# Kernel optimization log

Measured on AMD Instinct MI355X. Metric: run time of the kernel, lower is better.

## Reference

```python
import jax, jax.numpy as jnp
import numpy as np

N, K, D = 32768, 8192, 512
COMMITMENT_COST = 0.25

def setup_inputs() -> dict:
    key = jax.random.key(0)
    k1, k2 = jax.random.split(key)
    z = jax.random.normal(k1, (N, D), dtype=jnp.float32)
    # original inits uniform(-1/K, 1/K); scaled uniform keeps same distribution
    emb_weight = jax.random.uniform(k2, (K, D), dtype=jnp.float32, minval=-1.0 / K, maxval=1.0 / K)
    return {"z": z, "emb_weight": emb_weight}

def reference(z, emb_weight):
    z_flat = z.reshape(-1, emb_weight.shape[1])  # [N, D]
    # squared L2 distances: ||z||^2 + ||e||^2 - 2 z e^T  -> [N, K]
    distances = (
        jnp.sum(z_flat ** 2, axis=1, keepdims=True)
        + jnp.sum(emb_weight ** 2, axis=1)
        - 2.0 * jnp.matmul(z_flat, emb_weight.T)
    )
    code_indices = jnp.argmin(distances, axis=1)  # [N]
    quantized = emb_weight[code_indices]          # [N, D] gather
    e_latent_loss = jnp.mean((jax.lax.stop_gradient(quantized) - z_flat) ** 2)
    q_latent_loss = jnp.mean((quantized - jax.lax.stop_gradient(z_flat)) ** 2)
    loss = q_latent_loss + COMMITMENT_COST * e_latent_loss
    # straight-through estimator
    quantized_st = z_flat + jax.lax.stop_gradient(quantized - z_flat)
    return quantized_st, loss, code_indices
```

## Files before the change

kernel.cpp:

```cpp
#include <hip/hip_runtime.h>


#define N_ROWS 32768
#define K_CODES 8192
#define DIM 512

typedef __attribute__((ext_vector_type(8))) short short8;
typedef __attribute__((ext_vector_type(4))) float f32x4;

#define MARGIN 5e-4f

__device__ __forceinline__ unsigned short f2bf(float f) {
  unsigned int u = __float_as_uint(f);
  u = u + 0x7fffu + ((u >> 16) & 1u);
  return (unsigned short)(u >> 16);
}

__device__ __forceinline__ double shfl_xor_dbl(double v, int m) {
  union { double d; int i[2]; } u;
  u.d = v;
  u.i[0] = __shfl_xor(u.i[0], m, 64);
  u.i[1] = __shfl_xor(u.i[1], m, 64);
  return u.d;
}

__device__ __forceinline__ float opaque_f(float x) {
  asm volatile("" : "+v"(x));
  return x;
}

__global__ __launch_bounds__(256) void cvtnorm_k(
    const float* __restrict__ z, const float* __restrict__ e,
    unsigned short* __restrict__ zb, unsigned short* __restrict__ eb,
    float* __restrict__ a32, float* __restrict__ b32) {
  const int r = blockIdx.x * 4 + (threadIdx.x >> 6);
  const int lane = threadIdx.x & 63;
  const float* in; unsigned short* outb; float* outn; int rr;
  if (r < N_ROWS) { in = z; outb = zb; outn = a32; rr = r; }
  else            { in = e; outb = eb; outn = b32; rr = r - N_ROWS; }
  const float* xr = in + (size_t)rr * DIM + lane * 8;
  const float4 a = *(const float4*)xr;
  const float4 b = *(const float4*)(xr + 4);
  uint4 o;
  o.x = (unsigned)f2bf(a.x) | ((unsigned)f2bf(a.y) << 16);
  o.y = (unsigned)f2bf(a.z) | ((unsigned)f2bf(a.w) << 16);
  o.z = (unsigned)f2bf(b.x) | ((unsigned)f2bf(b.y) << 16);
  o.w = (unsigned)f2bf(b.z) | ((unsigned)f2bf(b.w) << 16);
  *(uint4*)(outb + (size_t)rr * DIM + lane * 8) = o;
  double s = (double)a.x * a.x + (double)a.y * a.y + (double)a.z * a.z + (double)a.w * a.w
           + (double)b.x * b.x + (double)b.y * b.y + (double)b.z * b.z + (double)b.w * b.w;
#pragma unroll
  for (int m = 1; m < 64; m <<= 1) s += shfl_xor_dbl(s, m);
  if (lane == 0) outn[rr] = (float)s;
}

__global__ __launch_bounds__(512, 4) void gemm_topk(
    const unsigned short* __restrict__ A,
    const unsigned short* __restrict__ B,
    const float* __restrict__ en2,
    float* __restrict__ candk,
    int* __restrict__ candi)
{
  __shared__ char lds[77824];
  float* scorebuf = (float*)lds;
  float* e2sAll = (float*)(lds + 73728);

  const int tid = threadIdx.x;
  const int lane = tid & 63, wave = tid >> 6;
  const int wm = wave >> 1, wn = wave & 1;
  const int quad = lane >> 4, lcol = lane & 15;
  const int bx = blockIdx.x >> 3, by = blockIdx.x & 7;
  const int row0 = bx * 256;
  const int cstart = by * 1024;
  const int hf = tid & 1, srow = tid >> 1;

  e2sAll[tid] = en2[cstart + tid];
  e2sAll[tid + 512] = en2[cstart + 512 + tid];

  float tk0 = 3.4e38f, tk1 = 3.4e38f, tk2 = 3.4e38f, tk3 = 3.4e38f;
  int ti0 = 0, ti1 = 0, ti2 = 0, ti3 = 0;

  const int schm = (lane & 3) ^ ((lane >> 3) & 3);
  const unsigned short* Ag =
      A + ((size_t)(row0 + wave * 32 + (lane >> 2))) * DIM + schm * 8;
  const int dstA = wave * 2048;
  const int dstB = 16384 + wave * 1024;

  const int swz = (quad ^ ((lcol >> 1) & 3)) * 16;
  int aoff[4], boff[4];
#pragma unroll
  for (int i = 0; i < 4; ++i) aoff[i] = (wm * 64 + i * 16 + lcol) * 64 + swz;
#pragma unroll
  for (int j = 0; j < 4; ++j) boff[j] = 16384 + (wn * 64 + j * 16 + lcol) * 64 + swz;

#define ASGP const __attribute__((address_space(1))) void*
#define LDSP __attribute__((address_space(3))) void*
#define STAGE(ktv, bb) do {                                                        \
    const unsigned short* As_ = Ag + (ktv) * 32;                                   \
    const unsigned short* Bs_ = Bg + (ktv) * 32;                                   \
    __builtin_amdgcn_global_load_lds((ASGP)(uintptr_t)(As_),                       \
        (LDSP)(uintptr_t)(lds + (bb) + dstA), 16, 0, 0);                           \
    __builtin_amdgcn_global_load_lds((ASGP)(uintptr_t)(As_ + 16 * DIM),            \
        (LDSP)(uintptr_t)(lds + (bb) + dstA + 1024), 16, 0, 0);                    \
    __builtin_amdgcn_global_load_lds((ASGP)(uintptr_t)(Bs_),                       \
        (LDSP)(uintptr_t)(lds + (bb) + dstB), 16, 0, 0);                           \
  } while (0)

#define COMPUTE(cbb) do {                                                          \
    short8 af[4], bv[4];                                                           \
    _Pragma("unroll")                                                              \
    for (int i = 0; i < 4; ++i) af[i] = *(const short8*)(lds + (cbb) + aoff[i]);   \
    _Pragma("unroll")                                                              \
    for (int j = 0; j < 4; ++j) bv[j] = *(const short8*)(lds + (cbb) + boff[j]);   \
    _Pragma("unroll")                                                              \
    for (int i = 0; i < 4; ++i)                                                    \
      _Pragma("unroll")                                                            \
      for (int j = 0; j < 4; ++j)                                                  \
        acc[i][j] = __builtin_amdgcn_mfma_f32_16x16x32_bf16(af[i], bv[j],          \
                                                            acc[i][j], 0, 0, 0);   \
  } while (0)

#pragma unroll 1
  for (int ct = 0; ct < 8; ++ct) {
    const int c0 = cstart + ct * 128;
    const unsigned short* Bg =
        B + ((size_t)(c0 + wave * 16 + (lane >> 2))) * DIM + schm * 8;

    f32x4 acc[4][4];
#pragma unroll
    for (int i = 0; i < 4; ++i)
#pragma unroll
      for (int j = 0; j < 4; ++j) acc[i][j] = 0.f;

    __syncthreads();
    STAGE(0, 0);
    STAGE(1, 24576);
    int cb = 0, nb = 24576, fb = 49152;
#pragma unroll 1
    for (int kt = 0; kt < 15; ++kt) {
      asm volatile("s_waitcnt vmcnt(3)" ::: "memory");
      __builtin_amdgcn_s_barrier();
      asm volatile("" ::: "memory");
      __builtin_amdgcn_sched_barrier(0);
      if (kt < 14) STAGE(kt + 2, fb);
      COMPUTE(cb);
      const int t = cb; cb = nb; nb = fb; fb = t;
    }
    asm volatile("s_waitcnt vmcnt(0)" ::: "memory");
    __builtin_amdgcn_s_barrier();
    asm volatile("" ::: "memory");
    __builtin_amdgcn_sched_barrier(0);
    COMPUTE(cb);

#pragma unroll 1
    for (int h = 0; h < 2; ++h) {
      __syncthreads();
      if (wn == h) {
#pragma unroll
        for (int i = 0; i < 4; ++i)
#pragma unroll
          for (int j = 0; j < 4; ++j) {
            const float eb2 = e2sAll[ct * 128 + 64 * h + 16 * j + lcol];
#pragma unroll
            for (int r = 0; r < 4; ++r)
              scorebuf[(wm * 64 + i * 16 + quad * 4 + r) * 67 + 16 * j + lcol] =
                  fmaf(acc[i][j][r], -2.0f, eb2);
          }
      }
      __syncthreads();
      const float* sp = scorebuf + srow * 67 + hf * 32;
      const int idbase = c0 + 64 * h + 32 * hf;
#pragma unroll 8
      for (int cc = 0; cc < 32; ++cc) {
        const float key = sp[cc];
        if (key < tk3) {
          const int id = idbase + cc;
          if (key < tk2) {
            tk3 = tk2; ti3 = ti2;
            if (key < tk1) {
              tk2 = tk1; ti2 = ti1;
              if (key < tk0) { tk1 = tk0; ti1 = ti0; tk0 = key; ti0 = id; }
              else           { tk1 = key; ti1 = id; }
            } else { tk2 = key; ti2 = id; }
          } else { tk3 = key; ti3 = id; }
        }
      }
    }
  }

  const size_t cb2 = ((size_t)(row0 + srow)) * 64 + by * 8 + hf * 4;
  candk[cb2 + 0] = tk0; candk[cb2 + 1] = tk1; candk[cb2 + 2] = tk2; candk[cb2 + 3] = tk3;
  candi[cb2 + 0] = ti0; candi[cb2 + 1] = ti1; candi[cb2 + 2] = ti2; candi[cb2 + 3] = ti3;
}

__global__ __launch_bounds__(256) void rescore_np(
    const float* __restrict__ z, const float* __restrict__ e,
    const float* __restrict__ a32, const float* __restrict__ b32,
    const float* __restrict__ candk, const int* __restrict__ candi,
    float* __restrict__ idxout)
{
  const int row = blockIdx.x * 4 + (threadIdx.x >> 6);
  const int lane = threadIdx.x & 63;

  const float myk = candk[(size_t)row * 64 + lane];
  float kmin = myk;
#pragma unroll
  for (int m = 1; m < 64; m <<= 1) kmin = fminf(kmin, __shfl_xor(kmin, m, 64));
  const float cut = kmin + MARGIN;

  float bd = 3.4e38f;
  int bc = 0x7fffffff;
  if (myk <= cut) {
    const int c = candi[(size_t)row * 64 + lane];
    const float* zr = z + (size_t)row * DIM;
    const float* er = e + (size_t)c * DIM;
    float s = 0.0f;
#pragma unroll 4
    for (int k4 = 0; k4 < 96; ++k4) {
      const float4 zv = *(const float4*)(zr + k4 * 4);
      const float4 ev = *(const float4*)(er + k4 * 4);
      s = fmaf(zv.x, ev.x, s);
      s = fmaf(zv.y, ev.y, s);
      s = fmaf(zv.z, ev.z, s);
      s = fmaf(zv.w, ev.w, s);
    }
    const float cA = s;
    s = 0.0f;
#pragma unroll 4
    for (int k4 = 96; k4 < 128; ++k4) {
      const float4 zv = *(const float4*)(zr + k4 * 4);
      const float4 ev = *(const float4*)(er + k4 * 4);
      s = fmaf(zv.x, ev.x, s);
      s = fmaf(zv.y, ev.y, s);
      s = fmaf(zv.z, ev.z, s);
      s = fmaf(zv.w, ev.w, s);
    }
    const float m = cA + s;
    const float t1 = a32[row] + b32[c];
    const float t2 = opaque_f(2.0f * m);
    bd = t1 - t2;
    bc = c;
  }
#pragma unroll
  for (int mm = 1; mm < 64; mm <<= 1) {
    const float od = __shfl_xor(bd, mm, 64);
    const int oc = __shfl_xor(bc, mm, 64);
    if (od < bd || (od == bd && oc < bc)) { bd = od; bc = oc; }
  }
  if (lane == 0) idxout[row] = (float)bc;
}

__global__ __launch_bounds__(256) void writeout_k(
    const float* __restrict__ z, const float* __restrict__ e,
    const float* __restrict__ idxf, float* __restrict__ outq,
    double* __restrict__ accum)
{
  const int tid = threadIdx.x;
  double s = 0.0;
  size_t gid = (size_t)blockIdx.x * 256 + tid;
#pragma unroll 1
  for (int it = 0; it < 16; ++it, gid += 262144) {
    const int row = (int)(gid >> 7);
    const int dq = ((int)gid & 127) << 2;
    const int c = (int)idxf[row];
    const float4 q4 = *(const float4*)(e + (size_t)c * DIM + dq);
    const float4 z4 = *(const float4*)(z + (size_t)row * DIM + dq);
    const float tx = q4.x - z4.x, ty = q4.y - z4.y, tz = q4.z - z4.z, tw = q4.w - z4.w;
    float4 o;
    o.x = z4.x + tx; o.y = z4.y + ty; o.z = z4.z + tz; o.w = z4.w + tw;
    *(float4*)(outq + (size_t)row * DIM + dq) = o;
    s += (double)tx * tx + (double)ty * ty + (double)tz * tz + (double)tw * tw;
  }
#pragma unroll
  for (int m = 1; m < 64; m <<= 1) s += shfl_xor_dbl(s, m);
  __shared__ double wsum[4];
  if ((tid & 63) == 0) wsum[tid >> 6] = s;
  __syncthreads();
  if (tid == 0) atomicAdd(accum, wsum[0] + wsum[1] + wsum[2] + wsum[3]);
}

__global__ void finalize_k(const double* __restrict__ accum, float* __restrict__ lossp) {
  *lossp = (float)(1.25 * accum[0] / (double)((size_t)N_ROWS * DIM));
}

extern "C" void kernel_launch(void* const* d_in, const int* in_sizes, int n_in,
                              void* d_out, int out_size, void* d_ws, size_t ws_size,
                              hipStream_t stream) {
  const float* z = (const float*)d_in[0];
  const float* e = (const float*)d_in[1];
  float* out = (float*)d_out;
  char* ob = (char*)d_out;

  unsigned short* zb = (unsigned short*)ob;
  unsigned short* eb = (unsigned short*)(ob + 33554432);
  float* b32   = (float*)(ob + 41943040);
  float* a32   = (float*)(ob + 41975808);
  float* candk = (float*)(ob + 42106880);
  int*   candi = (int*)(ob + 50495488);

  float* lossp = out + 16777216;
  float* idxs  = out + 16777217;
  double* accum = (double*)d_ws;

  hipMemsetAsync(d_ws, 0, sizeof(double), stream);
  cvtnorm_k<<<10240, 256, 0, stream>>>(z, e, zb, eb, a32, b32);
  gemm_topk<<<1024, 512, 0, stream>>>(zb, eb, b32, candk, candi);
  rescore_np<<<8192, 256, 0, stream>>>(z, e, a32, b32, candk, candi, idxs);
  writeout_k<<<1024, 256, 0, stream>>>(z, e, idxs, out, accum);
  finalize_k<<<1, 1, 0, stream>>>(accum, lossp);
}
```

Measured before the change: 784.9 us.

## Reshape GEMM tile to 128 rows x 256 codes and merge top-4 via shuffles

The fused GEMM+top-k kernel now uses a block tile of 128 rows by 256 codes instead of 256 by 128, with a 2x4 wave grid and twice as many blocks. Each row is scanned by four threads instead of two, each over 32 columns, and adjacent thread pairs then merge their top-4 lists with lane shuffles before a vectorized store. The intent is to shorten the serial per-thread top-k scan and raise block count for better occupancy or load balance. The cost is reloading A tiles across more blocks and a different LDS layout for the score buffer.

```diff
diff --git a/kernel.cpp b/kernel.cpp
--- a/kernel.cpp
+++ b/kernel.cpp
@@ -67,12 +67,12 @@
 
   const int tid = threadIdx.x;
   const int lane = tid & 63, wave = tid >> 6;
-  const int wm = wave >> 1, wn = wave & 1;
+  const int wm = wave >> 2, wn = wave & 3;
   const int quad = lane >> 4, lcol = lane & 15;
   const int bx = blockIdx.x >> 3, by = blockIdx.x & 7;
-  const int row0 = bx * 256;
+  const int row0 = bx * 128;
   const int cstart = by * 1024;
-  const int hf = tid & 1, srow = tid >> 1;
+  const int srow = tid >> 2, q = tid & 3;
 
   e2sAll[tid] = en2[cstart + tid];
   e2sAll[tid + 512] = en2[cstart + 512 + tid];
@@ -82,16 +82,16 @@
 
   const int schm = (lane & 3) ^ ((lane >> 3) & 3);
   const unsigned short* Ag =
-      A + ((size_t)(row0 + wave * 32 + (lane >> 2))) * DIM + schm * 8;
-  const int dstA = wave * 2048;
-  const int dstB = 16384 + wave * 1024;
+      A + ((size_t)(row0 + wave * 16 + (lane >> 2))) * DIM + schm * 8;
+  const int dstA = wave * 1024;
+  const int dstB = 8192 + wave * 2048;
 
   const int swz = (quad ^ ((lcol >> 1) & 3)) * 16;
   int aoff[4], boff[4];
 #pragma unroll
   for (int i = 0; i < 4; ++i) aoff[i] = (wm * 64 + i * 16 + lcol) * 64 + swz;
 #pragma unroll
-  for (int j = 0; j < 4; ++j) boff[j] = 16384 + (wn * 64 + j * 16 + lcol) * 64 + swz;
+  for (int j = 0; j < 4; ++j) boff[j] = 8192 + (wn * 64 + j * 16 + lcol) * 64 + swz;
 
 #define ASGP const __attribute__((address_space(1))) void*
 #define LDSP __attribute__((address_space(3))) void*
@@ -100,10 +100,10 @@
     const unsigned short* Bs_ = Bg + (ktv) * 32;                                   \
     __builtin_amdgcn_global_load_lds((ASGP)(uintptr_t)(As_),                       \
         (LDSP)(uintptr_t)(lds + (bb) + dstA), 16, 0, 0);                           \
-    __builtin_amdgcn_global_load_lds((ASGP)(uintptr_t)(As_ + 16 * DIM),            \
-        (LDSP)(uintptr_t)(lds + (bb) + dstA + 1024), 16, 0, 0);                    \
     __builtin_amdgcn_global_load_lds((ASGP)(uintptr_t)(Bs_),                       \
         (LDSP)(uintptr_t)(lds + (bb) + dstB), 16, 0, 0);                           \
+    __builtin_amdgcn_global_load_lds((ASGP)(uintptr_t)(Bs_ + 16 * DIM),            \
+        (LDSP)(uintptr_t)(lds + (bb) + dstB + 1024), 16, 0, 0);                    \
   } while (0)
 
 #define COMPUTE(cbb) do {                                                          \
@@ -120,11 +120,37 @@
                                                             acc[i][j], 0, 0, 0);   \
   } while (0)
 
+#define INS(sv, idv) do { \
+    if ((sv) < tk3) { \
+      const int id_ = (idv); \
+      if ((sv) < tk2) { \
+        tk3 = tk2; ti3 = ti2; \
+        if ((sv) < tk1) { \
+          tk2 = tk1; ti2 = ti1; \
+          if ((sv) < tk0) { tk1 = tk0; ti1 = ti0; tk0 = (sv); ti0 = id_; } \
+          else            { tk1 = (sv); ti1 = id_; } \
+        } else { tk2 = (sv); ti2 = id_; } \
+      } else { tk3 = (sv); ti3 = id_; } \
+    } \
+  } while (0)
+
+#define LTL(sv, idv, K, I) ((sv) < (K) || ((sv) == (K) && (idv) < (I)))
+#define INSM(sv, idv) do { \
+    if (LTL(sv, idv, tk3, ti3)) { \
+      if (LTL(sv, idv, tk2, ti2)) { tk3 = tk2; ti3 = ti2; \
+        if (LTL(sv, idv, tk1, ti1)) { tk2 = tk1; ti2 = ti1; \
+          if (LTL(sv, idv, tk0, ti0)) { tk1 = tk0; ti1 = ti0; tk0 = (sv); ti0 = (idv); } \
+          else { tk1 = (sv); ti1 = (idv); } \
+        } else { tk2 = (sv); ti2 = (idv); } \
+      } else { tk3 = (sv); ti3 = (idv); } \
+    } \
+  } while (0)
+
 #pragma unroll 1
-  for (int ct = 0; ct < 8; ++ct) {
-    const int c0 = cstart + ct * 128;
+  for (int ct = 0; ct < 4; ++ct) {
+    const int c0 = cstart + ct * 256;
     const unsigned short* Bg =
-        B + ((size_t)(c0 + wave * 16 + (lane >> 2))) * DIM + schm * 8;
+        B + ((size_t)(c0 + wave * 32 + (lane >> 2))) * DIM + schm * 8;
 
     f32x4 acc[4][4];
 #pragma unroll
@@ -155,42 +181,45 @@
 #pragma unroll 1
     for (int h = 0; h < 2; ++h) {
       __syncthreads();
-      if (wn == h) {
+      if ((wn >> 1) == h) {
 #pragma unroll
         for (int i = 0; i < 4; ++i)
 #pragma unroll
           for (int j = 0; j < 4; ++j) {
-            const float eb2 = e2sAll[ct * 128 + 64 * h + 16 * j + lcol];
+            const int colb = (wn & 1) * 64 + j * 16;
+            const float eb2 = e2sAll[ct * 256 + h * 128 + colb + lcol];
+            const int cidx = ((colb + lcol) >> 5) * 33 + ((colb & 31)) + lcol;
 #pragma unroll
             for (int r = 0; r < 4; ++r)
-              scorebuf[(wm * 64 + i * 16 + quad * 4 + r) * 67 + 16 * j + lcol] =
+              scorebuf[(wm * 64 + i * 16 + quad * 4 + r) * 132 + cidx] =
                   fmaf(acc[i][j][r], -2.0f, eb2);
           }
       }
       __syncthreads();
-      const float* sp = scorebuf + srow * 67 + hf * 32;
-      const int idbase = c0 + 64 * h + 32 * hf;
+      const float* sp = scorebuf + srow * 132 + q * 33;
+      const int idbase = c0 + h * 128 + q * 32;
 #pragma unroll 8
       for (int cc = 0; cc < 32; ++cc) {
         const float key = sp[cc];
-        if (key < tk3) {
-          const int id = idbase + cc;
-          if (key < tk2) {
-            tk3 = tk2; ti3 = ti2;
-            if (key < tk1) {
-              tk2 = tk1; ti2 = ti1;
-              if (key < tk0) { tk1 = tk0; ti1 = ti0; tk0 = key; ti0 = id; }
-              else           { tk1 = key; ti1 = id; }
-            } else { tk2 = key; ti2 = id; }
-          } else { tk3 = key; ti3 = id; }
-        }
+        if (key < tk3) INS(key, idbase + cc);
       }
     }
   }
 
-  const size_t cb2 = ((size_t)(row0 + srow)) * 64 + by * 8 + hf * 4;
-  candk[cb2 + 0] = tk0; candk[cb2 + 1] = tk1; candk[cb2 + 2] = tk2; candk[cb2 + 3] = tk3;
-  candi[cb2 + 0] = ti0; candi[cb2 + 1] = ti1; candi[cb2 + 2] = ti2; candi[cb2 + 3] = ti3;
+  {
+    float ok0 = __shfl_xor(tk0, 1, 64), ok1 = __shfl_xor(tk1, 1, 64);
+    float ok2 = __shfl_xor(tk2, 1, 64), ok3 = __shfl_xor(tk3, 1, 64);
+    int oi0 = __shfl_xor(ti0, 1, 64), oi1 = __shfl_xor(ti1, 1, 64);
+    int oi2 = __shfl_xor(ti2, 1, 64), oi3 = __shfl_xor(ti3, 1, 64);
+    INSM(ok0, oi0); INSM(ok1, oi1); INSM(ok2, oi2); INSM(ok3, oi3);
+  }
+  if ((q & 1) == 0) {
+    const size_t cb2 = ((size_t)(row0 + srow)) * 64 + by * 8 + (q >> 1) * 4;
+    float4 kf; kf.x = tk0; kf.y = tk1; kf.z = tk2; kf.w = tk3;
+    int4 fi; fi.x = ti0; fi.y = ti1; fi.z = ti2; fi.w = ti3;
+    *(float4*)(candk + cb2) = kf;
+    *(int4*)(candi + cb2) = fi;
+  }
 }
 
 __global__ __launch_bounds__(256) void rescore_np(
@@ -304,7 +333,7 @@
 
   hipMemsetAsync(d_ws, 0, sizeof(double), stream);
   cvtnorm_k<<<10240, 256, 0, stream>>>(z, e, zb, eb, a32, b32);
-  gemm_topk<<<1024, 512, 0, stream>>>(zb, eb, b32, candk, candi);
+  gemm_topk<<<2048, 512, 0, stream>>>(zb, eb, b32, candk, candi);
   rescore_np<<<8192, 256, 0, stream>>>(z, e, a32, b32, candk, candi, idxs);
   writeout_k<<<1024, 256, 0, stream>>>(z, e, idxs, out, accum);
   finalize_k<<<1, 1, 0, stream>>>(accum, lossp);
```

After: 770.0 us. No clear change (-1.9%).
